# Optimization experiments

Hardware: AMD Instinct MI355X
Metric: run time of the kernel (lower is better)

## Reference

```python
import jax, jax.numpy as jnp
import numpy as np

N, C_IN, C_OUT, T, V, K = 32, 64, 128, 300, 25, 3
EPS = 1e-5


def setup_inputs() -> dict:
    key = jax.random.key(0)
    ks = jax.random.split(key, 10)
    x = jax.random.normal(ks[0], (N, C_IN, T, V), dtype=jnp.float32)
    # fixed adjacency buffer (requires_grad=False in torch) and learned attention mask
    A = jax.random.uniform(ks[1], (K, V, V), dtype=jnp.float32)
    graph_attn = jnp.ones((K, V, V), dtype=jnp.float32)  # nn.init.constant_(1)
    # per-subset 1x1 conv weights/biases, stacked: [K, C_out, C_in]
    Wg = jax.random.normal(ks[2], (K, C_OUT, C_IN), dtype=jnp.float32) * np.sqrt(2.0 / (C_OUT * K))
    bg = jnp.zeros((K, C_OUT), dtype=jnp.float32)
    # main BN affine (torch init: weight=1e-6, bias=0; use small random for a nontrivial test)
    bn_gamma = jax.random.normal(ks[3], (C_OUT,), dtype=jnp.float32) * 0.1 + 1.0
    bn_beta = jax.random.normal(ks[4], (C_OUT,), dtype=jnp.float32) * 0.1
    # residual branch (in != out): 1x1 conv + BN
    Wr = jax.random.normal(ks[5], (C_OUT, C_IN), dtype=jnp.float32) * np.sqrt(2.0 / C_IN)
    br = jnp.zeros((C_OUT,), dtype=jnp.float32)
    rbn_gamma = jax.random.normal(ks[6], (C_OUT,), dtype=jnp.float32) * 0.1 + 1.0
    rbn_beta = jax.random.normal(ks[7], (C_OUT,), dtype=jnp.float32) * 0.1
    return {"x": x, "A": A, "graph_attn": graph_attn, "Wg": Wg, "bg": bg,
            "bn_gamma": bn_gamma, "bn_beta": bn_beta,
            "Wr": Wr, "br": br, "rbn_gamma": rbn_gamma, "rbn_beta": rbn_beta}


def _batchnorm(z, gamma, beta):
    # training-mode BatchNorm2d: biased batch stats over (N, T, V)
    mean = jnp.mean(z, axis=(0, 2, 3), keepdims=True)
    var = jnp.var(z, axis=(0, 2, 3), keepdims=True)
    zhat = (z - mean) * jax.lax.rsqrt(var + EPS)
    return zhat * gamma[None, :, None, None] + beta[None, :, None, None]


def reference(x, A, graph_attn, Wg, bg, bn_gamma, bn_beta, Wr, br, rbn_gamma, rbn_beta):
    Ae = A * graph_attn                                   # [K, V, V]
    # per-subset graph aggregation: (x.view(N, C*T, V) @ Ae[k])  -> [K, N, C, T, V]
    xA = jnp.einsum('nctv,kvw->knctw', x, Ae)
    # per-subset 1x1 conv then sum over subsets; biases sum as well
    hidden = jnp.einsum('knctv,koc->notv', xA, Wg) + jnp.sum(bg, axis=0)[None, :, None, None]
    hidden = _batchnorm(hidden, bn_gamma, bn_beta)
    # residual: 1x1 conv + BN (since in_channels != out_channels)
    res = jnp.einsum('nctv,oc->notv', x, Wr) + br[None, :, None, None]
    res = _batchnorm(res, rbn_gamma, rbn_beta)
    return hidden + res
```

## Files before the change

### kernel.cpp

```cpp
#include <hip/hip_runtime.h>

typedef __attribute__((ext_vector_type(8))) _Float16 half8;
typedef __attribute__((ext_vector_type(4))) _Float16 half4v;
typedef __attribute__((ext_vector_type(4))) float float4v;
typedef float float4u __attribute__((ext_vector_type(4), aligned(4)));
typedef unsigned long long u64;
typedef unsigned int u32;

#define NB   32
#define CIN  64
#define COUT 128
#define TT   300
#define VV   25
#define EPS  1e-5f
#define M_TOT 240000.0f
#define NBLK 1600

#define WS_WF    0
#define WS_AEF   65536
#define WS_ST    73728
#define WS_CF    75776
#define WS_WF2   77312
#define WS_TRASH 143360
#define WS_HR    1048576
#define WS_PARTP (WS_HR + 137625600)
#define WS_NEED  (WS_PARTP + 3276800)

__device__ __forceinline__ void bar_lds() {
    __builtin_amdgcn_sched_barrier(0);
    asm volatile("s_waitcnt lgkmcnt(0)" ::: "memory");
    __builtin_amdgcn_s_barrier();
    __builtin_amdgcn_sched_barrier(0);
}

__device__ __forceinline__ unsigned short f2h(float f) {
    return __builtin_bit_cast(unsigned short, (_Float16)f);
}
__device__ __forceinline__ float4v mfma16(half8 a, half8 b, float4v c) {
    return __builtin_amdgcn_mfma_f32_16x16x32_f16(a, b, c, 0, 0, 0);
}
__device__ __forceinline__ u32 pk2(float a, float b) {
    return __builtin_bit_cast(u32, __builtin_amdgcn_cvt_pkrtz(a, b));
}

__global__ void prep_kernel(const float* __restrict__ A, const float* __restrict__ ga,
                            const float* __restrict__ Wg, const float* __restrict__ Wr,
                            char* __restrict__ wsb) {
    unsigned short* wf = (unsigned short*)(wsb + WS_WF);
    unsigned short* ae = (unsigned short*)(wsb + WS_AEF);
    float* st = (float*)(wsb + WS_ST);
    int i = blockIdx.x * blockDim.x + threadIdx.x;
    for (; i < 32768 + 4096 + 512; i += gridDim.x * blockDim.x) {
        if (i < 32768) {
            int on = i >> 12, kt = (i >> 9) & 7, l = (i >> 3) & 63, j = i & 7;
            int o = on * 16 + (l & 15);
            int kc = kt * 32 + ((l >> 4) << 3) + j;
            float v = (kc < 192) ? Wg[((kc >> 6) * COUT + o) * CIN + (kc & 63)]
                                 : Wr[o * CIN + (kc - 192)];
            wf[i] = f2h(v);
        } else if (i < 32768 + 4096) {
            int q = i - 32768;
            int k = q >> 10, nt = (q >> 9) & 1, l = (q >> 3) & 63, j = q & 7;
            int v = ((l >> 4) << 3) + j, w = nt * 16 + (l & 15);
            float val = 0.0f;
            if (v < VV && w < VV)
                val = (k < 3) ? A[(k * VV + v) * VV + w] * ga[(k * VV + v) * VV + w]
                              : (v == w ? 1.0f : 0.0f);
            ae[q] = f2h(val);
        } else {
            st[i - 36864] = 0.0f;
        }
    }
}

__global__ __launch_bounds__(256) void red_kernel(const float* __restrict__ part,
                                                  char* __restrict__ wsb) {
    float* st = (float*)(wsb + WS_ST);
    __shared__ float red[4][4];
    const int tid = threadIdx.x, wv = tid >> 6, lane = tid & 63;
    const int i0 = blockIdx.x * 4;
    const int bi = tid >> 2, ii = tid & 3;
    float s = 0.0f;
    for (int b = bi; b < NBLK; b += 64)
        s += part[(size_t)b * 512 + i0 + ii];
    s += __shfl_xor(s, 4);
    s += __shfl_xor(s, 8);
    s += __shfl_xor(s, 16);
    s += __shfl_xor(s, 32);
    if (lane < 4) red[wv][lane] = s;
    __syncthreads();
    if (tid < 4) st[i0 + tid] = red[0][tid] + red[1][tid] + red[2][tid] + red[3][tid];
}

__global__ __launch_bounds__(256) void scale_kernel(
        const float* __restrict__ Wg, const float* __restrict__ Wr,
        const float* __restrict__ g1, const float* __restrict__ b1,
        const float* __restrict__ g2, const float* __restrict__ b2,
        char* __restrict__ wsb, int fillw2) {
    const float* st = (const float*)(wsb + WS_ST);
    float* cf = (float*)(wsb + WS_CF);
    unsigned short* wf2 = (unsigned short*)(wsb + WS_WF2);
    __shared__ float cl[384];
    int tid = threadIdx.x;
    if (tid < 128) {
        int o = tid;
        const float inv_m = 1.0f / M_TOT;
        float mH = st[o] * inv_m,        vH = st[128 + o] * inv_m - mH * mH;
        float mR = st[256 + o] * inv_m,  vR = st[384 + o] * inv_m - mR * mR;
        float scH = g1[o] * rsqrtf(vH + EPS);
        float scR = g2[o] * rsqrtf(vR + EPS);
        float bC  = b1[o] + b2[o] - scH * mH - scR * mR;
        cl[o] = scH; cl[128 + o] = scR; cl[256 + o] = bC;
        if (blockIdx.x == 0) { cf[o] = scH; cf[128 + o] = scR; cf[256 + o] = bC; }
    }
    __syncthreads();
    if (!fillw2) return;
    for (int i = blockIdx.x * 256 + tid; i < 32768; i += gridDim.x * 256) {
        int on = i >> 12, kt = (i >> 9) & 7, l = (i >> 3) & 63, j = i & 7;
        int o = on * 16 + (l & 15);
        int kc = kt * 32 + ((l >> 4) << 3) + j;
        float v = (kc < 192) ? Wg[((kc >> 6) * COUT + o) * CIN + (kc & 63)] * cl[o]
                             : Wr[o * CIN + (kc - 192)] * cl[128 + o];
        wf2[i] = f2h(v);
    }
}

template <int MODE>
__global__ __launch_bounds__(256, 2) void gcn_kernel(
        const float* __restrict__ x, char* __restrict__ wsb, float* __restrict__ out,
        float* __restrict__ part) {
    __shared__ __align__(16) _Float16 xa[64 * 256];
    __shared__ __align__(16) _Float16 xs[2][64][32];
    char* xab = (char*)xa;

    const unsigned short* wf = (const unsigned short*)(wsb + (MODE == 1 ? WS_WF2 : WS_WF));
    const unsigned short* ae = (const unsigned short*)(wsb + WS_AEF);
    const float* cf = (const float*)(wsb + WS_CF);

    const int tid = threadIdx.x, wv = tid >> 6, l = tid & 63;
    const int l15 = l & 15, lq = l >> 4;

    half8 af[2][8];
#pragma unroll
    for (int on = 0; on < 2; ++on)
#pragma unroll
        for (int kt = 0; kt < 8; ++kt)
            af[on][kt] = *(const half8*)&wf[(((wv * 2 + on) * 8 + kt) * 64 + l) * 8];

    half8 aef[4][2];
#pragma unroll
    for (int k = 0; k < 4; ++k)
#pragma unroll
        for (int nt = 0; nt < 2; ++nt)
            aef[k][nt] = *(const half8*)&ae[((k * 2 + nt) * 64 + l) * 8];

    float bC2[2];
    if (MODE == 1) {
#pragma unroll
        for (int on = 0; on < 2; ++on)
            bC2[on] = cf[256 + wv * 32 + on * 16 + l15];
    }

    float sH[2], sH2[2], sR[2], sR2[2];
    if (MODE != 1) {
#pragma unroll
        for (int on = 0; on < 2; ++on) { sH[on] = 0; sH2[on] = 0; sR[on] = 0; sR2[on] = 0; }
    }

    for (int e = tid; e < 896; e += 256) {
        int t = e / 448, r = e % 448;
        xs[t][r / 7][25 + r % 7] = (_Float16)0.0f;
    }

    float4v pre[4];
    auto issue_pre = [&](int n_, int t0_) {
#pragma unroll
        for (int p = 0; p < 4; ++p) {
            int idx = tid + p * 256;
            int c = idx >> 4, i = idx & 15;
            int f0 = i * 4; f0 = f0 > 46 ? 46 : f0;
            const float* g = x + n_ * 480000 + c * 7500 + t0_ * 25 + f0;
            float4u v = *(const float4u*)g;
            pre[p][0] = v[0]; pre[p][1] = v[1]; pre[p][2] = v[2]; pre[p][3] = v[3];
        }
    };
    auto write_xs = [&]() {
#pragma unroll
        for (int p = 0; p < 4; ++p) {
            int idx = tid + p * 256;
            int c = idx >> 4, i = idx & 15;
            int f0 = i * 4; f0 = f0 > 46 ? 46 : f0;
#pragma unroll
            for (int s = 0; s < 4; ++s) {
                int f = f0 + s;
                int tsel = (f >= 25) ? 1 : 0;
                xs[tsel][c][f - tsel * 25] = (_Float16)pre[p][s];
            }
        }
    };

    const int tile0 = blockIdx.x * 3;
    { int n0 = tile0 / 150, t00 = (tile0 % 150) * 2; issue_pre(n0, t00); }
    write_xs();

    for (int it = 0; it < 3; ++it) {
        const int tile = tile0 + it;
        const int n = tile / 150, t0 = (tile % 150) * 2;
        bar_lds();

        const bool hn = (it < 2);
        if (hn) { int tl = tile + 1; issue_pre(tl / 150, (tl % 150) * 2); }

#pragma unroll
        for (int t = 0; t < 2; ++t) {
            half8 xf = *(const half8*)&xs[t][wv * 16 + l15][lq * 8];
#pragma unroll
            for (int k = 0; k < 4; ++k)
#pragma unroll
                for (int nt = 0; nt < 2; ++nt) {
                    float4v c4 = {0.0f, 0.0f, 0.0f, 0.0f};
                    c4 = mfma16(xf, aef[k][nt], c4);
                    int col = t * 32 + nt * 16 + l15;
                    int kcb = (k * 64 + wv * 16 + lq * 4) * 2;
                    u64 pk = ((u64)pk2(c4[2], c4[3]) << 32) | pk2(c4[0], c4[1]);
                    *(u64*)(xab + ((col << 9) + (kcb ^ ((col & 7) << 4)))) = pk;
                }
        }
        bar_lds();

        float4v acc[4][2];
        if (MODE != 1) {
#pragma unroll
            for (int cm = 0; cm < 4; ++cm)
#pragma unroll
                for (int on = 0; on < 2; ++on) acc[cm][on] = {0.0f, 0.0f, 0.0f, 0.0f};
#pragma unroll
            for (int kt = 0; kt < 6; ++kt)
#pragma unroll
                for (int cm = 0; cm < 4; ++cm) {
                    int col = cm * 16 + l15;
                    half8 bf = *(const half8*)(xab + ((col << 9) +
                                   ((kt * 64 + lq * 16) ^ ((col & 7) << 4))));
                    acc[cm][0] = mfma16(bf, af[0][kt], acc[cm][0]);
                    acc[cm][1] = mfma16(bf, af[1][kt], acc[cm][1]);
                }
#pragma unroll
            for (int cm = 0; cm < 4; ++cm)
#pragma unroll
                for (int on = 0; on < 2; ++on) {
#pragma unroll
                    for (int r = 0; r < 4; ++r) {
                        float h = acc[cm][on][r];
                        sH[on] += h; sH2[on] += h * h;
                    }
                    if (MODE == 2) {
                        int t = t0 + (cm >> 1);
                        int o = wv * 32 + on * 16 + l15;
                        size_t off = WS_HR + (size_t)((n * COUT + o) * TT + t) * 112
                                   + (cm & 1) * 32 + lq * 8;
                        if (cm & 1) off = (lq == 3) ? (size_t)WS_TRASH : off;
                        u32 p0 = pk2(acc[cm][on][0], acc[cm][on][1]);
                        u32 p1 = pk2(acc[cm][on][2], acc[cm][on][3]);
                        *(u64*)(wsb + off) = ((u64)p1 << 32) | p0;
                    }
                    acc[cm][on] = {0.0f, 0.0f, 0.0f, 0.0f};
                }
#pragma unroll
            for (int kt = 6; kt < 8; ++kt)
#pragma unroll
                for (int cm = 0; cm < 4; ++cm) {
                    int col = cm * 16 + l15;
                    half8 bf = *(const half8*)(xab + ((col << 9) +
                                   ((kt * 64 + lq * 16) ^ ((col & 7) << 4))));
                    acc[cm][0] = mfma16(bf, af[0][kt], acc[cm][0]);
                    acc[cm][1] = mfma16(bf, af[1][kt], acc[cm][1]);
                }
#pragma unroll
            for (int cm = 0; cm < 4; ++cm)
#pragma unroll
                for (int on = 0; on < 2; ++on) {
#pragma unroll
                    for (int r = 0; r < 4; ++r) {
                        float rv = acc[cm][on][r];
                        sR[on] += rv; sR2[on] += rv * rv;
                    }
                    if (MODE == 2) {
                        int t = t0 + (cm >> 1);
                        int o = wv * 32 + on * 16 + l15;
                        size_t off = WS_HR + (size_t)((n * COUT + o) * TT + t) * 112 + 56
                                   + (cm & 1) * 32 + lq * 8;
                        if (cm & 1) off = (lq == 3) ? (size_t)WS_TRASH : off;
                        u32 p0 = pk2(acc[cm][on][0], acc[cm][on][1]);
                        u32 p1 = pk2(acc[cm][on][2], acc[cm][on][3]);
                        *(u64*)(wsb + off) = ((u64)p1 << 32) | p0;
                    }
                }
        } else {
#pragma unroll
            for (int cm = 0; cm < 4; ++cm)
#pragma unroll
                for (int on = 0; on < 2; ++on)
#pragma unroll
                    for (int r = 0; r < 4; ++r) acc[cm][on][r] = bC2[on];
#pragma unroll
            for (int kt = 0; kt < 8; ++kt)
#pragma unroll
                for (int cm = 0; cm < 4; ++cm) {
                    int col = cm * 16 + l15;
                    half8 bf = *(const half8*)(xab + ((col << 9) +
                                   ((kt * 64 + lq * 16) ^ ((col & 7) << 4))));
                    acc[cm][0] = mfma16(bf, af[0][kt], acc[cm][0]);
                    acc[cm][1] = mfma16(bf, af[1][kt], acc[cm][1]);
                }
#pragma unroll
            for (int cm = 0; cm < 4; ++cm) {
                int t = t0 + (cm >> 1);
#pragma unroll
                for (int on = 0; on < 2; ++on) {
                    int o = wv * 32 + on * 16 + l15;
                    float* op = out + ((size_t)(n * COUT + o) * TT + t) * VV;
                    if (!(cm & 1)) {
                        *(float4u*)(op + lq * 4) = acc[cm][on];
                    } else if (lq < 2) {
                        *(float4u*)(op + 16 + lq * 4) = acc[cm][on];
                    } else if (lq == 2) {
                        op[24] = acc[cm][on][0];
                    }
                }
            }
        }

        if (hn) write_xs();
    }

    if (MODE != 1) {
#pragma unroll
        for (int on = 0; on < 2; ++on) {
            sH[on]  += __shfl_xor(sH[on], 16);  sH[on]  += __shfl_xor(sH[on], 32);
            sH2[on] += __shfl_xor(sH2[on], 16); sH2[on] += __shfl_xor(sH2[on], 32);
            sR[on]  += __shfl_xor(sR[on], 16);  sR[on]  += __shfl_xor(sR[on], 32);
            sR2[on] += __shfl_xor(sR2[on], 16); sR2[on] += __shfl_xor(sR2[on], 32);
        }
        if (l < 16) {
            float* pb = part + (size_t)blockIdx.x * 512;
#pragma unroll
            for (int on = 0; on < 2; ++on) {
                int o = wv * 32 + on * 16 + l15;
                pb[o]       = sH[on];
                pb[128 + o] = sH2[on];
                pb[256 + o] = sR[on];
                pb[384 + o] = sR2[on];
            }
        }
    }
}

__global__ __launch_bounds__(256) void bn_apply(const char* __restrict__ wsb,
                                                float* __restrict__ out) {
    const float* cf = (const float*)(wsb + WS_CF);
    const int total = 1228800 * 7;
    for (int j = blockIdx.x * 256 + threadIdx.x; j < total; j += gridDim.x * 256) {
        int row = j / 7;
        int q = j - row * 7;
        int o = (row / 300) & 127;
        float scH = cf[o], scR = cf[128 + o], bC = cf[256 + o];
        const char* rp = wsb + WS_HR + (size_t)row * 112;
        u64 hh = *(const u64*)(rp + q * 8);
        u64 rr = *(const u64*)(rp + 56 + q * 8);
        half4v h4 = __builtin_bit_cast(half4v, hh);
        half4v r4 = __builtin_bit_cast(half4v, rr);
        float* op = out + (size_t)row * 25 + q * 4;
        if (q < 6) {
            float4u v;
#pragma unroll
            for (int k = 0; k < 4; ++k)
                v[k] = scH * (float)h4[k] + scR * (float)r4[k] + bC;
            *(float4u*)op = v;
        } else {
            op[0] = scH * (float)h4[0] + scR * (float)r4[0] + bC;
        }
    }
}

extern "C" void kernel_launch(void* const* d_in, const int* in_sizes, int n_in,
                              void* d_out, int out_size, void* d_ws, size_t ws_size,
                              hipStream_t stream) {
    const float* x        = (const float*)d_in[0];
    const float* A        = (const float*)d_in[1];
    const float* ga       = (const float*)d_in[2];
    const float* Wg       = (const float*)d_in[3];
    const float* bn_gamma = (const float*)d_in[5];
    const float* bn_beta  = (const float*)d_in[6];
    const float* Wr       = (const float*)d_in[7];
    const float* rbn_g    = (const float*)d_in[9];
    const float* rbn_b    = (const float*)d_in[10];
    char* wsb  = (char*)d_ws;
    float* out = (float*)d_out;

    const bool primary = ws_size >= (size_t)WS_NEED + 4096;
    float* partP = (float*)(wsb + WS_PARTP);
    float* partF = (float*)(wsb + WS_HR);

    prep_kernel<<<64, 256, 0, stream>>>(A, ga, Wg, Wr, wsb);
    if (primary) {
        gcn_kernel<2><<<NBLK, 256, 0, stream>>>(x, wsb, nullptr, partP);
        red_kernel<<<128, 256, 0, stream>>>(partP, wsb);
        scale_kernel<<<64, 256, 0, stream>>>(Wg, Wr, bn_gamma, bn_beta, rbn_g, rbn_b, wsb, 0);
        bn_apply<<<2048, 256, 0, stream>>>(wsb, out);
    } else {
        gcn_kernel<0><<<NBLK, 256, 0, stream>>>(x, wsb, nullptr, partF);
        red_kernel<<<128, 256, 0, stream>>>(partF, wsb);
        scale_kernel<<<64, 256, 0, stream>>>(Wg, Wr, bn_gamma, bn_beta, rbn_g, rbn_b, wsb, 1);
        gcn_kernel<1><<<NBLK, 256, 0, stream>>>(x, wsb, out, partF);
    }
}
```

Before: 139.8 us.

## Stage x tiles directly into LDS via global_load_lds with swizzled fp32 layout

Replaces the register-prefetch-then-LDS-write staging of x with direct global-to-LDS loads (global_load_lds), storing fp32 rows in an XOR-swizzled layout and converting to fp16 at MFMA operand load time. The next tile's prefetch is now issued after the aggregation barrier and waited on with vmcnt at loop end, removing the per-element register round trip and the convert-and-scatter writes. The tradeoff is a larger LDS footprint (fp32 instead of fp16), conversion work on the read side, and a hand-tuned vmcnt wait that must match the number of outstanding loads (MODE 2 leaves 16 in flight).

New measurement: 148.1 us. 5.9% more time.

```diff
diff --git a/kernel.cpp b/kernel.cpp
--- a/kernel.cpp
+++ b/kernel.cpp
@@ -3,6 +3,7 @@
 typedef __attribute__((ext_vector_type(8))) _Float16 half8;
 typedef __attribute__((ext_vector_type(4))) _Float16 half4v;
 typedef __attribute__((ext_vector_type(4))) float float4v;
+typedef __attribute__((ext_vector_type(4))) unsigned int uint4v;
 typedef float float4u __attribute__((ext_vector_type(4), aligned(4)));
 typedef unsigned long long u64;
 typedef unsigned int u32;
@@ -25,6 +26,9 @@
 #define WS_HR    1048576
 #define WS_PARTP (WS_HR + 137625600)
 #define WS_NEED  (WS_PARTP + 3276800)
+
+typedef const __attribute__((address_space(1))) u32 gld_t;
+typedef __attribute__((address_space(3))) u32 lds_t;
 
 __device__ __forceinline__ void bar_lds() {
     __builtin_amdgcn_sched_barrier(0);
@@ -130,7 +134,7 @@
         const float* __restrict__ x, char* __restrict__ wsb, float* __restrict__ out,
         float* __restrict__ part) {
     __shared__ __align__(16) _Float16 xa[64 * 256];
-    __shared__ __align__(16) _Float16 xs[2][64][32];
+    __shared__ __align__(16) float xsf[2][64][32];
     char* xab = (char*)xa;
 
     const unsigned short* wf = (const unsigned short*)(wsb + (MODE == 1 ? WS_WF2 : WS_WF));
@@ -167,53 +171,40 @@
         for (int on = 0; on < 2; ++on) { sH[on] = 0; sH2[on] = 0; sR[on] = 0; sR2[on] = 0; }
     }
 
-    for (int e = tid; e < 896; e += 256) {
-        int t = e / 448, r = e % 448;
-        xs[t][r / 7][25 + r % 7] = (_Float16)0.0f;
-    }
-
-    float4v pre[4];
-    auto issue_pre = [&](int n_, int t0_) {
-#pragma unroll
-        for (int p = 0; p < 4; ++p) {
-            int idx = tid + p * 256;
-            int c = idx >> 4, i = idx & 15;
-            int f0 = i * 4; f0 = f0 > 46 ? 46 : f0;
-            const float* g = x + n_ * 480000 + c * 7500 + t0_ * 25 + f0;
-            float4u v = *(const float4u*)g;
-            pre[p][0] = v[0]; pre[p][1] = v[1]; pre[p][2] = v[2]; pre[p][3] = v[3];
+    auto stage_glds = [&](int n_, int t0_) {
+#pragma unroll
+        for (int i = 0; i < 16; ++i) {
+            int j = wv * 16 + i;
+            int t = j >> 5, cc = j & 31;
+            int c = cc * 2 + (l >> 5);
+            int qd = (((l & 31) >> 2) ^ (c & 7));
+            int v = qd * 4 + (l & 3);
+            if (v > 24) v = 24;
+            const float* src = x + n_ * 480000 + c * 7500 + (t0_ + t) * 25 + v;
+            lds_t* dst = (lds_t*)&xsf[t][cc * 2][0];
+            __builtin_amdgcn_global_load_lds((gld_t*)src, dst, 4, 0, 0);
         }
     };
-    auto write_xs = [&]() {
-#pragma unroll
-        for (int p = 0; p < 4; ++p) {
-            int idx = tid + p * 256;
-            int c = idx >> 4, i = idx & 15;
-            int f0 = i * 4; f0 = f0 > 46 ? 46 : f0;
-#pragma unroll
-            for (int s = 0; s < 4; ++s) {
-                int f = f0 + s;
-                int tsel = (f >= 25) ? 1 : 0;
-                xs[tsel][c][f - tsel * 25] = (_Float16)pre[p][s];
-            }
-        }
-    };
 
     const int tile0 = blockIdx.x * 3;
-    { int n0 = tile0 / 150, t00 = (tile0 % 150) * 2; issue_pre(n0, t00); }
-    write_xs();
+    { int n0 = tile0 / 150, t00 = (tile0 % 150) * 2; stage_glds(n0, t00); }
+    __builtin_amdgcn_sched_barrier(0);
+    asm volatile("s_waitcnt vmcnt(0) lgkmcnt(0)" ::: "memory");
+    __builtin_amdgcn_s_barrier();
+    __builtin_amdgcn_sched_barrier(0);
 
     for (int it = 0; it < 3; ++it) {
         const int tile = tile0 + it;
         const int n = tile / 150, t0 = (tile % 150) * 2;
-        bar_lds();
-
-        const bool hn = (it < 2);
-        if (hn) { int tl = tile + 1; issue_pre(tl / 150, (tl % 150) * 2); }
 
 #pragma unroll
         for (int t = 0; t < 2; ++t) {
-            half8 xf = *(const half8*)&xs[t][wv * 16 + l15][lq * 8];
+            int c = wv * 16 + l15;
+            const float* rowp = &xsf[t][c][0];
+            float4u a = *(const float4u*)(rowp + ((((lq * 2)    ) ^ (c & 7)) << 2));
+            float4u b = *(const float4u*)(rowp + ((((lq * 2) + 1) ^ (c & 7)) << 2));
+            uint4v uw = {pk2(a[0], a[1]), pk2(a[2], a[3]), pk2(b[0], b[1]), pk2(b[2], b[3])};
+            half8 xf = __builtin_bit_cast(half8, uw);
 #pragma unroll
             for (int k = 0; k < 4; ++k)
 #pragma unroll
@@ -227,6 +218,9 @@
                 }
         }
         bar_lds();
+
+        const bool hn = (it < 2);
+        if (hn) { int tl = tile + 1; stage_glds(tl / 150, (tl % 150) * 2); }
 
         float4v acc[4][2];
         if (MODE != 1) {
@@ -330,7 +324,13 @@
             }
         }
 
-        if (hn) write_xs();
+        if (hn) {
+            __builtin_amdgcn_sched_barrier(0);
+            if (MODE == 2) asm volatile("s_waitcnt vmcnt(16) lgkmcnt(0)" ::: "memory");
+            else           asm volatile("s_waitcnt vmcnt(0) lgkmcnt(0)" ::: "memory");
+            __builtin_amdgcn_s_barrier();
+            __builtin_amdgcn_sched_barrier(0);
+        }
     }
 
     if (MODE != 1) {
```

## Stage fp16 intermediates through LDS for coalesced tiled workspace writes and reads

Applied to the files above, without the earlier changes.

The gcn kernel now computes the hidden and residual accumulators together, then transposes them through LDS so each thread writes one contiguous 112-byte row. This replaces the scattered 8-byte global stores and the trash-address trick. The workspace becomes tile-major, and bn_apply is rewritten as one block per tile with simple contiguous per-thread reads instead of a grid-stride loop using divisions. The cost is an extra LDS round trip with two barriers per tile, and more live accumulator registers.

Measured after the change: 203.2 us. 45.3% more time.

```diff
diff --git a/kernel.cpp b/kernel.cpp
--- a/kernel.cpp
+++ b/kernel.cpp
@@ -3,7 +3,10 @@
 typedef __attribute__((ext_vector_type(8))) _Float16 half8;
 typedef __attribute__((ext_vector_type(4))) _Float16 half4v;
 typedef __attribute__((ext_vector_type(4))) float float4v;
+typedef __attribute__((ext_vector_type(4))) unsigned int uint4v;
+typedef unsigned int uint4u __attribute__((ext_vector_type(4), aligned(4)));
 typedef float float4u __attribute__((ext_vector_type(4), aligned(4)));
+typedef float float2u __attribute__((ext_vector_type(2), aligned(4)));
 typedef unsigned long long u64;
 typedef unsigned int u32;
 
@@ -15,13 +18,13 @@
 #define EPS  1e-5f
 #define M_TOT 240000.0f
 #define NBLK 1600
+#define NTILE 4800
 
 #define WS_WF    0
 #define WS_AEF   65536
 #define WS_ST    73728
 #define WS_CF    75776
 #define WS_WF2   77312
-#define WS_TRASH 143360
 #define WS_HR    1048576
 #define WS_PARTP (WS_HR + 137625600)
 #define WS_NEED  (WS_PARTP + 3276800)
@@ -228,90 +231,84 @@
         }
         bar_lds();
 
-        float4v acc[4][2];
+        float4v accH[4][2], accR[4][2];
+#pragma unroll
+        for (int cm = 0; cm < 4; ++cm)
+#pragma unroll
+            for (int on = 0; on < 2; ++on) {
+                accH[cm][on] = {0.0f, 0.0f, 0.0f, 0.0f};
+                accR[cm][on] = {0.0f, 0.0f, 0.0f, 0.0f};
+            }
+#pragma unroll
+        for (int kt = 0; kt < 8; ++kt)
+#pragma unroll
+            for (int cm = 0; cm < 4; ++cm) {
+                int col = cm * 16 + l15;
+                half8 bf = *(const half8*)(xab + ((col << 9) +
+                               ((kt * 64 + lq * 16) ^ ((col & 7) << 4))));
+                if (kt < 6) {
+                    accH[cm][0] = mfma16(bf, af[0][kt], accH[cm][0]);
+                    accH[cm][1] = mfma16(bf, af[1][kt], accH[cm][1]);
+                } else {
+                    accR[cm][0] = mfma16(bf, af[0][kt], accR[cm][0]);
+                    accR[cm][1] = mfma16(bf, af[1][kt], accR[cm][1]);
+                }
+            }
+
         if (MODE != 1) {
 #pragma unroll
             for (int cm = 0; cm < 4; ++cm)
 #pragma unroll
-                for (int on = 0; on < 2; ++on) acc[cm][on] = {0.0f, 0.0f, 0.0f, 0.0f};
-#pragma unroll
-            for (int kt = 0; kt < 6; ++kt)
-#pragma unroll
-                for (int cm = 0; cm < 4; ++cm) {
-                    int col = cm * 16 + l15;
-                    half8 bf = *(const half8*)(xab + ((col << 9) +
-                                   ((kt * 64 + lq * 16) ^ ((col & 7) << 4))));
-                    acc[cm][0] = mfma16(bf, af[0][kt], acc[cm][0]);
-                    acc[cm][1] = mfma16(bf, af[1][kt], acc[cm][1]);
-                }
-#pragma unroll
-            for (int cm = 0; cm < 4; ++cm)
-#pragma unroll
-                for (int on = 0; on < 2; ++on) {
+                for (int on = 0; on < 2; ++on)
 #pragma unroll
                     for (int r = 0; r < 4; ++r) {
-                        float h = acc[cm][on][r];
+                        float h = accH[cm][on][r], rv = accR[cm][on][r];
                         sH[on] += h; sH2[on] += h * h;
-                    }
-                    if (MODE == 2) {
-                        int t = t0 + (cm >> 1);
-                        int o = wv * 32 + on * 16 + l15;
-                        size_t off = WS_HR + (size_t)((n * COUT + o) * TT + t) * 112
-                                   + (cm & 1) * 32 + lq * 8;
-                        if (cm & 1) off = (lq == 3) ? (size_t)WS_TRASH : off;
-                        u32 p0 = pk2(acc[cm][on][0], acc[cm][on][1]);
-                        u32 p1 = pk2(acc[cm][on][2], acc[cm][on][3]);
-                        *(u64*)(wsb + off) = ((u64)p1 << 32) | p0;
-                    }
-                    acc[cm][on] = {0.0f, 0.0f, 0.0f, 0.0f};
-                }
-#pragma unroll
-            for (int kt = 6; kt < 8; ++kt)
-#pragma unroll
-                for (int cm = 0; cm < 4; ++cm) {
-                    int col = cm * 16 + l15;
-                    half8 bf = *(const half8*)(xab + ((col << 9) +
-                                   ((kt * 64 + lq * 16) ^ ((col & 7) << 4))));
-                    acc[cm][0] = mfma16(bf, af[0][kt], acc[cm][0]);
-                    acc[cm][1] = mfma16(bf, af[1][kt], acc[cm][1]);
-                }
-#pragma unroll
-            for (int cm = 0; cm < 4; ++cm)
-#pragma unroll
-                for (int on = 0; on < 2; ++on) {
-#pragma unroll
-                    for (int r = 0; r < 4; ++r) {
-                        float rv = acc[cm][on][r];
                         sR[on] += rv; sR2[on] += rv * rv;
                     }
-                    if (MODE == 2) {
-                        int t = t0 + (cm >> 1);
-                        int o = wv * 32 + on * 16 + l15;
-                        size_t off = WS_HR + (size_t)((n * COUT + o) * TT + t) * 112 + 56
-                                   + (cm & 1) * 32 + lq * 8;
-                        if (cm & 1) off = (lq == 3) ? (size_t)WS_TRASH : off;
-                        u32 p0 = pk2(acc[cm][on][0], acc[cm][on][1]);
-                        u32 p1 = pk2(acc[cm][on][2], acc[cm][on][3]);
-                        *(u64*)(wsb + off) = ((u64)p1 << 32) | p0;
-                    }
+        }
+
+        if (MODE == 2) {
+            bar_lds();
+#pragma unroll
+            for (int cm = 0; cm < 4; ++cm)
+#pragma unroll
+                for (int on = 0; on < 2; ++on) {
+                    int o = wv * 32 + on * 16 + l15;
+                    int c = (cm >> 1) * 64 + (cm & 1) * 32 + lq * 8;
+                    int swc = c ^ ((o & 7) << 4);
+                    u64 hp = (u64)pk2(accH[cm][on][0], accH[cm][on][1]) |
+                             ((u64)pk2(accH[cm][on][2], accH[cm][on][3]) << 32);
+                    u64 rp = (u64)pk2(accR[cm][on][0], accR[cm][on][1]) |
+                             ((u64)pk2(accR[cm][on][2], accR[cm][on][3]) << 32);
+                    *(u64*)(xab + o * 128 + swc) = hp;
+                    *(u64*)(xab + 16384 + o * 128 + swc) = rp;
                 }
-        } else {
-#pragma unroll
-            for (int cm = 0; cm < 4; ++cm)
-#pragma unroll
-                for (int on = 0; on < 2; ++on)
-#pragma unroll
-                    for (int r = 0; r < 4; ++r) acc[cm][on][r] = bC2[on];
-#pragma unroll
-            for (int kt = 0; kt < 8; ++kt)
-#pragma unroll
-                for (int cm = 0; cm < 4; ++cm) {
-                    int col = cm * 16 + l15;
-                    half8 bf = *(const half8*)(xab + ((col << 9) +
-                                   ((kt * 64 + lq * 16) ^ ((col & 7) << 4))));
-                    acc[cm][0] = mfma16(bf, af[0][kt], acc[cm][0]);
-                    acc[cm][1] = mfma16(bf, af[1][kt], acc[cm][1]);
-                }
+            bar_lds();
+            {
+                int o = tid >> 1, t = tid & 1;
+                int sw = (o & 7) << 4;
+                const char* rowH = xab + o * 128;
+                const char* rowR = xab + 16384 + o * 128;
+                uint4v h0 = *(const uint4v*)(rowH + ((t * 64 +  0) ^ sw));
+                uint4v h1 = *(const uint4v*)(rowH + ((t * 64 + 16) ^ sw));
+                uint4v h2 = *(const uint4v*)(rowH + ((t * 64 + 32) ^ sw));
+                u64    h3 = *(const u64*)  (rowH + ((t * 64 + 48) ^ sw));
+                uint4v r0 = *(const uint4v*)(rowR + ((t * 64 +  0) ^ sw));
+                uint4v r1 = *(const uint4v*)(rowR + ((t * 64 + 16) ^ sw));
+                uint4v r2 = *(const uint4v*)(rowR + ((t * 64 + 32) ^ sw));
+                u64    r3 = *(const u64*)  (rowR + ((t * 64 + 48) ^ sw));
+                char* dst = wsb + WS_HR + (size_t)tile * 28672 + tid * 112;
+                *(uint4v*)(dst +  0) = h0;
+                *(uint4v*)(dst + 16) = h1;
+                *(uint4v*)(dst + 32) = h2;
+                *(u64*)  (dst + 48) = h3;
+                *(uint4u*)(dst + 56) = r0;
+                *(uint4u*)(dst + 72) = r1;
+                *(uint4u*)(dst + 88) = r2;
+                *(u64*)  (dst + 104) = r3;
+            }
+        } else if (MODE == 1) {
 #pragma unroll
             for (int cm = 0; cm < 4; ++cm) {
                 int t = t0 + (cm >> 1);
@@ -319,12 +316,16 @@
                 for (int on = 0; on < 2; ++on) {
                     int o = wv * 32 + on * 16 + l15;
                     float* op = out + ((size_t)(n * COUT + o) * TT + t) * VV;
+                    float4u vv;
+#pragma unroll
+                    for (int r = 0; r < 4; ++r)
+                        vv[r] = accH[cm][on][r] + accR[cm][on][r] + bC2[on];
                     if (!(cm & 1)) {
-                        *(float4u*)(op + lq * 4) = acc[cm][on];
+                        *(float4u*)(op + lq * 4) = vv;
                     } else if (lq < 2) {
-                        *(float4u*)(op + 16 + lq * 4) = acc[cm][on];
+                        *(float4u*)(op + 16 + lq * 4) = vv;
                     } else if (lq == 2) {
-                        op[24] = acc[cm][on][0];
+                        op[24] = vv[0];
                     }
                 }
             }
@@ -358,27 +359,27 @@
 __global__ __launch_bounds__(256) void bn_apply(const char* __restrict__ wsb,
                                                 float* __restrict__ out) {
     const float* cf = (const float*)(wsb + WS_CF);
-    const int total = 1228800 * 7;
-    for (int j = blockIdx.x * 256 + threadIdx.x; j < total; j += gridDim.x * 256) {
-        int row = j / 7;
-        int q = j - row * 7;
-        int o = (row / 300) & 127;
-        float scH = cf[o], scR = cf[128 + o], bC = cf[256 + o];
-        const char* rp = wsb + WS_HR + (size_t)row * 112;
-        u64 hh = *(const u64*)(rp + q * 8);
-        u64 rr = *(const u64*)(rp + 56 + q * 8);
-        half4v h4 = __builtin_bit_cast(half4v, hh);
-        half4v r4 = __builtin_bit_cast(half4v, rr);
-        float* op = out + (size_t)row * 25 + q * 4;
-        if (q < 6) {
-            float4u v;
-#pragma unroll
-            for (int k = 0; k < 4; ++k)
-                v[k] = scH * (float)h4[k] + scR * (float)r4[k] + bC;
-            *(float4u*)op = v;
-        } else {
-            op[0] = scH * (float)h4[0] + scR * (float)r4[0] + bC;
-        }
+    const int tile = blockIdx.x;
+    const int n = tile / 150, t0 = (tile % 150) * 2;
+    const int tid = threadIdx.x;
+    const int o = tid >> 1, t = tid & 1;
+    const float scH = cf[o], scR = cf[128 + o], bC = cf[256 + o];
+    const char* rp = wsb + WS_HR + (size_t)tile * 28672 + tid * 112;
+    float* op = out + ((size_t)(n * COUT + o) * TT + (t0 + t)) * VV;
+#pragma unroll
+    for (int q = 0; q < 6; ++q) {
+        half4v h4 = *(const half4v*)(rp + q * 8);
+        half4v r4 = *(const half4v*)(rp + 56 + q * 8);
+        float4u v;
+#pragma unroll
+        for (int k = 0; k < 4; ++k)
+            v[k] = scH * (float)h4[k] + scR * (float)r4[k] + bC;
+        *(float4u*)(op + q * 4) = v;
+    }
+    {
+        half4v h4 = *(const half4v*)(rp + 48);
+        half4v r4 = *(const half4v*)(rp + 56 + 48);
+        op[24] = scH * (float)h4[0] + scR * (float)r4[0] + bC;
     }
 }
 
@@ -406,7 +407,7 @@
         gcn_kernel<2><<<NBLK, 256, 0, stream>>>(x, wsb, nullptr, partP);
         red_kernel<<<128, 256, 0, stream>>>(partP, wsb);
         scale_kernel<<<64, 256, 0, stream>>>(Wg, Wr, bn_gamma, bn_beta, rbn_g, rbn_b, wsb, 0);
-        bn_apply<<<2048, 256, 0, stream>>>(wsb, out);
+        bn_apply<<<NTILE, 256, 0, stream>>>(wsb, out);
     } else {
         gcn_kernel<0><<<NBLK, 256, 0, stream>>>(x, wsb, nullptr, partF);
         red_kernel<<<128, 256, 0, stream>>>(partF, wsb);
```

## Store fp16 intermediates in tile-contiguous layout and stage bn_apply through LDS

Applied to the files above, without the earlier changes.

The GEMM kernel now writes its fp16 hidden and residual intermediates in a per-tile contiguous layout that follows the MFMA fragment order, replacing the strided per-row scatter and its trash-slot writes. bn_apply becomes one block per tile that copies the 28 KB tile into LDS with coalesced loads, then remaps entries to output positions. An extra barrier with a partial vmcnt wait is added at the end of each loop iteration. The aim is to cut scattered global writes and reads, at the cost of LDS traffic and index arithmetic in bn_apply, and it relies on the new tile layout matching on both sides.

New measurement: 120.4 us (median of 2 runs). 1.16x faster.

```diff
diff --git a/kernel.cpp b/kernel.cpp
--- a/kernel.cpp
+++ b/kernel.cpp
@@ -15,13 +15,13 @@
 #define EPS  1e-5f
 #define M_TOT 240000.0f
 #define NBLK 1600
+#define NTILE 4800
 
 #define WS_WF    0
 #define WS_AEF   65536
 #define WS_ST    73728
 #define WS_CF    75776
 #define WS_WF2   77312
-#define WS_TRASH 143360
 #define WS_HR    1048576
 #define WS_PARTP (WS_HR + 137625600)
 #define WS_NEED  (WS_PARTP + 3276800)
@@ -41,6 +41,10 @@
 }
 __device__ __forceinline__ u32 pk2(float a, float b) {
     return __builtin_bit_cast(u32, __builtin_amdgcn_cvt_pkrtz(a, b));
+}
+__device__ __forceinline__ int hr_off(int cm, int on) {
+    return (cm & 1) ? (2048 + (cm >> 1) * 768 + on * 384)
+                    : ((cm >> 1) * 1024 + on * 512);
 }
 
 __global__ void prep_kernel(const float* __restrict__ A, const float* __restrict__ ga,
@@ -228,6 +232,8 @@
         }
         bar_lds();
 
+        char* hrw = wsb + WS_HR + (size_t)tile * 28672 + wv * 7168;
+
         float4v acc[4][2];
         if (MODE != 1) {
 #pragma unroll
@@ -254,14 +260,13 @@
                         sH[on] += h; sH2[on] += h * h;
                     }
                     if (MODE == 2) {
-                        int t = t0 + (cm >> 1);
-                        int o = wv * 32 + on * 16 + l15;
-                        size_t off = WS_HR + (size_t)((n * COUT + o) * TT + t) * 112
-                                   + (cm & 1) * 32 + lq * 8;
-                        if (cm & 1) off = (lq == 3) ? (size_t)WS_TRASH : off;
-                        u32 p0 = pk2(acc[cm][on][0], acc[cm][on][1]);
-                        u32 p1 = pk2(acc[cm][on][2], acc[cm][on][3]);
-                        *(u64*)(wsb + off) = ((u64)p1 << 32) | p0;
+                        u64 p = (u64)pk2(acc[cm][on][0], acc[cm][on][1]) |
+                                ((u64)pk2(acc[cm][on][2], acc[cm][on][3]) << 32);
+                        if (!(cm & 1)) {
+                            *(u64*)(hrw + hr_off(cm, on) + l * 8) = p;
+                        } else if (lq < 3) {
+                            *(u64*)(hrw + hr_off(cm, on) + l * 8) = p;
+                        }
                     }
                     acc[cm][on] = {0.0f, 0.0f, 0.0f, 0.0f};
                 }
@@ -285,14 +290,13 @@
                         sR[on] += rv; sR2[on] += rv * rv;
                     }
                     if (MODE == 2) {
-                        int t = t0 + (cm >> 1);
-                        int o = wv * 32 + on * 16 + l15;
-                        size_t off = WS_HR + (size_t)((n * COUT + o) * TT + t) * 112 + 56
-                                   + (cm & 1) * 32 + lq * 8;
-                        if (cm & 1) off = (lq == 3) ? (size_t)WS_TRASH : off;
-                        u32 p0 = pk2(acc[cm][on][0], acc[cm][on][1]);
-                        u32 p1 = pk2(acc[cm][on][2], acc[cm][on][3]);
-                        *(u64*)(wsb + off) = ((u64)p1 << 32) | p0;
+                        u64 p = (u64)pk2(acc[cm][on][0], acc[cm][on][1]) |
+                                ((u64)pk2(acc[cm][on][2], acc[cm][on][3]) << 32);
+                        if (!(cm & 1)) {
+                            *(u64*)(hrw + 3584 + hr_off(cm, on) + l * 8) = p;
+                        } else if (lq < 3) {
+                            *(u64*)(hrw + 3584 + hr_off(cm, on) + l * 8) = p;
+                        }
                     }
                 }
         } else {
@@ -331,6 +335,14 @@
         }
 
         if (hn) write_xs();
+
+        if (it < 2) {
+            __builtin_amdgcn_sched_barrier(0);
+            if (MODE == 2) asm volatile("s_waitcnt vmcnt(16) lgkmcnt(0)" ::: "memory");
+            else           asm volatile("s_waitcnt vmcnt(0) lgkmcnt(0)" ::: "memory");
+            __builtin_amdgcn_s_barrier();
+            __builtin_amdgcn_sched_barrier(0);
+        }
     }
 
     if (MODE != 1) {
@@ -357,19 +369,35 @@
 
 __global__ __launch_bounds__(256) void bn_apply(const char* __restrict__ wsb,
                                                 float* __restrict__ out) {
+    __shared__ u64 lds[3584];
     const float* cf = (const float*)(wsb + WS_CF);
-    const int total = 1228800 * 7;
-    for (int j = blockIdx.x * 256 + threadIdx.x; j < total; j += gridDim.x * 256) {
-        int row = j / 7;
-        int q = j - row * 7;
-        int o = (row / 300) & 127;
+    const int tile = blockIdx.x;
+    const int n = tile / 150, t0 = (tile % 150) * 2;
+    const int tid = threadIdx.x;
+
+    const u64* src = (const u64*)(wsb + WS_HR + (size_t)tile * 28672);
+#pragma unroll
+    for (int i = 0; i < 14; ++i) lds[tid + i * 256] = src[tid + i * 256];
+    __syncthreads();
+
+#pragma unroll
+    for (int i = 0; i < 7; ++i) {
+        int j2 = tid + i * 256;
+        int row = j2 / 7, q = j2 - row * 7;
+        int o = row >> 1, t = row & 1;
+        int v0 = (q < 6) ? q * 4 : 24;
+        int cm = t * 2 + (v0 >> 4);
+        int lq = (v0 & 15) >> 2;
+        int ll = lq * 16 + (o & 15);
+        int wv = o >> 5, on = (o >> 4) & 1;
+        int offq = (cm & 1) ? (256 + (cm >> 1) * 96 + on * 48)
+                            : ((cm >> 1) * 128 + on * 64);
+        u64 h64 = lds[wv * 896 + offq + ll];
+        u64 r64 = lds[wv * 896 + 448 + offq + ll];
+        half4v h4 = __builtin_bit_cast(half4v, h64);
+        half4v r4 = __builtin_bit_cast(half4v, r64);
         float scH = cf[o], scR = cf[128 + o], bC = cf[256 + o];
-        const char* rp = wsb + WS_HR + (size_t)row * 112;
-        u64 hh = *(const u64*)(rp + q * 8);
-        u64 rr = *(const u64*)(rp + 56 + q * 8);
-        half4v h4 = __builtin_bit_cast(half4v, hh);
-        half4v r4 = __builtin_bit_cast(half4v, rr);
-        float* op = out + (size_t)row * 25 + q * 4;
+        float* op = out + ((size_t)(n * COUT + o) * TT + t0 + t) * VV + v0;
         if (q < 6) {
             float4u v;
 #pragma unroll
@@ -406,7 +434,7 @@
         gcn_kernel<2><<<NBLK, 256, 0, stream>>>(x, wsb, nullptr, partP);
         red_kernel<<<128, 256, 0, stream>>>(partP, wsb);
         scale_kernel<<<64, 256, 0, stream>>>(Wg, Wr, bn_gamma, bn_beta, rbn_g, rbn_b, wsb, 0);
-        bn_apply<<<2048, 256, 0, stream>>>(wsb, out);
+        bn_apply<<<NTILE, 256, 0, stream>>>(wsb, out);
     } else {
         gcn_kernel<0><<<NBLK, 256, 0, stream>>>(x, wsb, nullptr, partF);
         red_kernel<<<128, 256, 0, stream>>>(partF, wsb);
```
